# Performance work log

Measured on AMD Instinct MI355X. Metric: run time of the kernel, lower is better.

Reference implementation:

```python
import jax, jax.numpy as jnp
import numpy as np

B, N, D = 1024, 32, 512  # graphs, node types (=nodes per graph), node_dim
EPS = 1e-5

def setup_inputs() -> dict:
    key = jax.random.key(0)
    ks = jax.random.split(key, 6)
    z = jax.random.normal(ks[0], (B, N, D), jnp.float32)
    # each graph contains every node type exactly once, in random order
    idx = jax.vmap(lambda k: jax.random.permutation(k, N))(jax.random.split(ks[1], B)).astype(jnp.int32)
    A = jax.random.normal(ks[2], (N, N), jnp.float32) / np.sqrt(N)
    W1 = jax.random.normal(ks[3], (N, D, 2 * D), jnp.float32) / np.sqrt(D)
    b1 = jnp.zeros((N, 2 * D), jnp.float32)
    W2 = jax.random.normal(ks[4], (N, 2 * D, D), jnp.float32) / np.sqrt(2 * D)
    b2 = jnp.zeros((N, D), jnp.float32)
    gamma = jnp.ones((D,), jnp.float32)
    beta = jnp.zeros((D,), jnp.float32)
    return dict(z=z, idx=idx, A=A, W1=W1, b1=b1, W2=W2, b2=b2, gamma=gamma, beta=beta)

def _layernorm(x, g, b):
    m = jnp.mean(x, axis=-1, keepdims=True)
    v = jnp.var(x, axis=-1, keepdims=True)
    return (x - m) * jax.lax.rsqrt(v + EPS) * g + b

def reference(z, idx, A, W1, b1, W2, b2, gamma, beta):
    # per-graph submatrix of global A: A_sub[b] = A[node_index, node_index]
    A_sub = A[idx[:, :, None], idx[:, None, :]]            # [B,K,K]
    # Az[b] = A_sub[b].T @ z[b]
    Az = jnp.einsum('bkj,bkd->bjd', A_sub, z)              # [B,K,D]
    Az = _layernorm(Az, gamma, beta)
    # route node of type t to expert t: inv[b,t] = position of type t in graph b
    inv = jnp.argsort(idx, axis=1)                         # [B,N]
    x = jnp.take_along_axis(Az, inv[:, :, None], axis=1)   # [B,N,D] type-ordered
    # per-type 2-layer MLP experts (Linear -> ELU -> Linear), dropout in eval mode
    h = jax.nn.elu(jnp.einsum('bnd,ndh->bnh', x, W1) + b1) # [B,N,2D]
    y = jnp.einsum('bnh,nhd->bnd', h, W2) + b2             # [B,N,D]
    # scatter back to node order: node j in graph b has type idx[b,j]
    mix = jnp.take_along_axis(y, idx[:, :, None].astype(jnp.int32), axis=1)
    return mix + Az
```

## Files before the change

### kernel.cpp

```cpp
#include <hip/hip_runtime.h>
#include <hip/hip_bf16.h>
#include <math.h>

#define B_  1024
#define N_  32
#define D_  512
#define EPS_ 1e-5f

typedef __attribute__((ext_vector_type(8))) short bf16x8;
typedef __attribute__((ext_vector_type(4))) float f32x4;
using bf16 = __hip_bfloat16;
typedef unsigned int u32;
typedef const u32 __attribute__((address_space(1)))* gp_t;
typedef u32 __attribute__((address_space(3)))* sp_t;

static __device__ __forceinline__ void gload16(const void* g, void* s) {
  __builtin_amdgcn_global_load_lds((gp_t)g, (sp_t)s, 16, 0, 0);
}
static __device__ __forceinline__ void bar() {
  asm volatile("s_barrier" ::: "memory");
}

static __device__ __forceinline__ unsigned short f2bf(float f) {
  union { float f; u32 u; } c; c.f = f;
  u32 r = c.u + 0x7fff + ((c.u >> 16) & 1);
  return (unsigned short)(r >> 16);
}
static __device__ __forceinline__ float bf2f(unsigned short h) {
  union { u32 u; float f; } c; c.u = ((u32)h) << 16;
  return c.f;
}

__global__ __launch_bounds__(256) void transpose_cast_kernel(
    const float* __restrict__ in, bf16* __restrict__ out, int R, int C) {
  __shared__ unsigned short tile[64][65];
  const size_t mat = (size_t)blockIdx.z * (size_t)R * (size_t)C;
  const float* inp = in + mat;
  bf16* outp = out + mat;
  const int c0 = blockIdx.x * 64, r0 = blockIdx.y * 64;
  const int tr = threadIdx.x >> 4;
  const int tc = (threadIdx.x & 15) * 4;
#pragma unroll
  for (int i = 0; i < 4; ++i) {
    const int r = tr + i * 16;
    float4 v = *(const float4*)&inp[(size_t)(r0 + r) * C + c0 + tc];
    tile[r][tc + 0] = f2bf(v.x);
    tile[r][tc + 1] = f2bf(v.y);
    tile[r][tc + 2] = f2bf(v.z);
    tile[r][tc + 3] = f2bf(v.w);
  }
  __syncthreads();
#pragma unroll
  for (int i = 0; i < 2; ++i) {
    const int chunk = i * 256 + threadIdx.x;
    const int c = chunk >> 3, r8 = (chunk & 7) * 8;
    union { bf16x8 v; unsigned short u[8]; } pk;
#pragma unroll
    for (int k = 0; k < 8; ++k) pk.u[k] = tile[r8 + k][c];
    *(bf16x8*)&outp[(size_t)(c0 + c) * R + r0 + r8] = pk.v;
  }
}

__global__ __launch_bounds__(512) void mix_ln_kernel(
    const float* __restrict__ z, const int* __restrict__ idx,
    const float* __restrict__ A, const float* __restrict__ gamma,
    const float* __restrict__ beta, bf16* __restrict__ x_ws,
    int* __restrict__ inv_ws) {
  __shared__ float As[32][32];
  __shared__ int   p[32];
  __shared__ float red1[8][32];
  __shared__ float red2[8][32];
  __shared__ float meanS[32];
  __shared__ float rstdS[32];

  const int b = blockIdx.x;
  const int t = threadIdx.x;
  const int lane = t & 63, wid = t >> 6;

  if (t < 32) {
    int v = idx[b * 32 + t];
    p[t] = v;
    inv_ws[b * 32 + v] = t;
  }
  __syncthreads();
#pragma unroll
  for (int i = 0; i < 2; ++i) {
    const int id = i * 512 + t;
    As[id >> 5][id & 31] = A[p[id >> 5] * 32 + (id & 31)];
  }
  __syncthreads();

  const float* zb = z + (size_t)b * (N_ * D_) + t;
  float acc[32];
#pragma unroll
  for (int n = 0; n < 32; ++n) acc[n] = 0.f;

  float zr[8];
#pragma unroll 1
  for (int q = 0; q < 4; ++q) {
#pragma unroll
    for (int kk = 0; kk < 8; ++kk) zr[kk] = zb[(q * 8 + kk) * D_];
#pragma unroll
    for (int kk = 0; kk < 8; ++kk) {
      const int k = q * 8 + kk;
      const float zv = zr[kk];
#pragma unroll
      for (int c = 0; c < 8; ++c) {
        float4 a4 = *(const float4*)&As[k][c * 4];
        acc[c * 4 + 0] = fmaf(a4.x, zv, acc[c * 4 + 0]);
        acc[c * 4 + 1] = fmaf(a4.y, zv, acc[c * 4 + 1]);
        acc[c * 4 + 2] = fmaf(a4.z, zv, acc[c * 4 + 2]);
        acc[c * 4 + 3] = fmaf(a4.w, zv, acc[c * 4 + 3]);
      }
    }
  }

#pragma unroll
  for (int n = 0; n < 32; ++n) {
    float v1 = acc[n];
    float v2 = acc[n] * acc[n];
#pragma unroll
    for (int mk = 1; mk < 64; mk <<= 1) {
      v1 += __shfl_xor(v1, mk);
      v2 += __shfl_xor(v2, mk);
    }
    if (lane == 0) { red1[wid][n] = v1; red2[wid][n] = v2; }
  }
  __syncthreads();
  if (t < 32) {
    float S1 = 0.f, S2 = 0.f;
#pragma unroll
    for (int w = 0; w < 8; ++w) { S1 += red1[w][t]; S2 += red2[w][t]; }
    float mean = S1 * (1.f / D_);
    float var  = S2 * (1.f / D_) - mean * mean;
    meanS[t] = mean;
    rstdS[t] = rsqrtf(var + EPS_);
  }
  __syncthreads();

  const float g = gamma[t], be = beta[t];
#pragma unroll
  for (int n = 0; n < 32; ++n) {
    float x0 = (acc[n] - meanS[n]) * rstdS[n] * g + be;
    x_ws[((size_t)n * B_ + b) * D_ + t] = __float2bfloat16(x0);
  }
}

#define STG_A(P, H, S) do {                                                   \
    const bf16* g_ = Ag + (size_t)((H) * 128) * KD + (S) * 64 + soff;         \
    gload16(g_, Alds + (P) * 32768 + (H) * 16384 + dof);                      \
    gload16(g_ + (size_t)64 * KD, Alds + (P) * 32768 + (H) * 16384 + 8192 + dof); \
  } while (0)
#define STG_B(P, H, S) do {                                                   \
    const bf16* g_ = Bg + (size_t)((H) * 128) * KD + (S) * 64 + soff;         \
    gload16(g_, Blds + (P) * 32768 + (H) * 16384 + dof);                      \
    gload16(g_ + (size_t)64 * KD, Blds + (P) * 32768 + (H) * 16384 + 8192 + dof); \
  } while (0)

#define RD_A(P, H) do {                                                       \
    const char* Ab_ = Alds + (P) * 32768 + (H) * 16384;                       \
    _Pragma("unroll")                                                         \
    for (int fi = 0; fi < 2; ++fi) {                                          \
      av[fi][0] = *(const bf16x8*)(Ab_ + raA + fi * 2048 + j16);              \
      av[fi][1] = *(const bf16x8*)(Ab_ + raA + fi * 2048 + (j16 ^ 64));       \
    }                                                                         \
  } while (0)
#define RD_B(P, H, BV) do {                                                   \
    const char* Bb_ = Blds + (P) * 32768 + (H) * 16384;                       \
    _Pragma("unroll")                                                         \
    for (int fj = 0; fj < 4; ++fj) {                                          \
      BV[fj][0] = *(const bf16x8*)(Bb_ + raB + fj * 2048 + j16);              \
      BV[fj][1] = *(const bf16x8*)(Bb_ + raB + fj * 2048 + (j16 ^ 64));       \
    }                                                                         \
  } while (0)

#define MMA16(QR, QC, BV) do {                                                \
    __builtin_amdgcn_s_setprio(1);                                            \
    _Pragma("unroll")                                                         \
    for (int fi = 0; fi < 2; ++fi)                                            \
      _Pragma("unroll")                                                       \
      for (int fj = 0; fj < 4; ++fj) {                                        \
        acc[QR][QC][fi][fj] = __builtin_amdgcn_mfma_f32_16x16x32_bf16(        \
            av[fi][0], BV[fj][0], acc[QR][QC][fi][fj], 0, 0, 0);              \
        acc[QR][QC][fi][fj] = __builtin_amdgcn_mfma_f32_16x16x32_bf16(        \
            av[fi][1], BV[fj][1], acc[QR][QC][fi][fj], 0, 0, 0);              \
      }                                                                       \
    __builtin_amdgcn_s_setprio(0);                                            \
  } while (0)

#define VMC4() asm volatile("s_waitcnt vmcnt(4)" ::: "memory")
#define VMC0() asm volatile("s_waitcnt vmcnt(0)" ::: "memory")

template <int KD, int NS>
static __device__ __forceinline__ void gemm8_core(
    const bf16* __restrict__ Ag, const bf16* __restrict__ Bg,
    char* __restrict__ Alds, char* __restrict__ Blds,
    f32x4 (&acc)[2][2][2][4], const int t) {
  const int lane = t & 63, wid = t >> 6;
  const int llo = lane & 15, lhi = lane >> 4;
  const int raA = ((wid & 3) * 32 + llo) * 128;
  const int raB = ((wid >> 2) * 64 + llo) * 128;
  const int j16 = (lhi ^ (llo & 7)) * 16;
  const int soff = (t >> 3) * KD + ((t ^ (t >> 3)) & 7) * 8;
  const int dof = wid * 1024;

  bf16x8 av[2][2], bv0[4][2], bv1[4][2];

  STG_A(0, 0, 0); STG_B(0, 0, 0); STG_A(0, 1, 0); STG_B(0, 1, 0);
  STG_A(1, 0, 1); STG_B(1, 0, 1);
  VMC4();
  bar();

#pragma unroll 1
  for (int it = 0; it < NS / 2; ++it) {
    const int s0 = 2 * it;
    RD_A(0, 0); RD_B(0, 0, bv0);
    if (s0 + 1 < NS) STG_A(1, 1, s0 + 1);
    bar(); MMA16(0, 0, bv0); bar();
    RD_B(0, 1, bv1);
    if (s0 + 1 < NS) STG_B(1, 1, s0 + 1);
    bar(); MMA16(0, 1, bv1); bar();
    RD_A(0, 1);
    if (s0 + 2 < NS) STG_A(0, 0, s0 + 2);
    bar(); MMA16(1, 1, bv1); bar();
    if (s0 + 2 < NS) STG_B(0, 0, s0 + 2);
    bar(); MMA16(1, 0, bv0);
    if (s0 + 2 < NS) { VMC4(); } else { VMC0(); }
    bar();
    const int s1 = s0 + 1;
    RD_A(1, 0); RD_B(1, 0, bv0);
    if (s1 + 1 < NS) STG_A(0, 1, s1 + 1);
    bar(); MMA16(0, 0, bv0); bar();
    RD_B(1, 1, bv1);
    if (s1 + 1 < NS) STG_B(0, 1, s1 + 1);
    bar(); MMA16(0, 1, bv1); bar();
    RD_A(1, 1);
    if (s1 + 2 < NS) STG_A(1, 0, s1 + 2);
    bar(); MMA16(1, 1, bv1); bar();
    if (s1 + 2 < NS) STG_B(1, 0, s1 + 2);
    bar(); MMA16(1, 0, bv0);
    if (s1 + 2 < NS) { VMC4(); } else { VMC0(); }
    bar();
  }
}

__global__ __launch_bounds__(512, 2) void gemm1_kernel(
    const bf16* __restrict__ X,
    const bf16* __restrict__ W1t,
    const float* __restrict__ b1,
    bf16* __restrict__ Hout) {
  extern __shared__ char lds[];
  char* Alds = lds;
  char* Blds = lds + 65536;

  const int bid = blockIdx.x;
  const int swz = (bid & 7) * 64 + (bid >> 3);
  const int m  = swz >> 4;
  const int r_ = swz & 15;
  const int hb = r_ >> 2, bb = r_ & 3;

  const int t = threadIdx.x;
  const int lane = t & 63, wid = t >> 6;
  const int llo = lane & 15, lhi = lane >> 4;

  const bf16* Ag = W1t + (size_t)m * (1024 * 512) + (size_t)(hb * 256) * 512;
  const bf16* Bg = X   + (size_t)m * (1024 * 512) + (size_t)(bb * 256) * 512;

  const f32x4 fzero = {0.f, 0.f, 0.f, 0.f};
  f32x4 acc[2][2][2][4];
#pragma unroll
  for (int a = 0; a < 2; ++a)
#pragma unroll
    for (int b = 0; b < 2; ++b)
#pragma unroll
      for (int c = 0; c < 2; ++c)
#pragma unroll
        for (int d = 0; d < 4; ++d) acc[a][b][c][d] = fzero;

  gemm8_core<512, 8>(Ag, Bg, Alds, Blds, acc, t);

  const float* b1m = b1 + m * 1024 + hb * 256;
#pragma unroll
  for (int qr = 0; qr < 2; ++qr)
#pragma unroll
    for (int fi = 0; fi < 2; ++fi) {
      const int h_loc = qr * 128 + (wid & 3) * 32 + fi * 16 + lhi * 4;
      const float4 bi = *(const float4*)&b1m[h_loc];
#pragma unroll
      for (int qc = 0; qc < 2; ++qc)
#pragma unroll
        for (int fj = 0; fj < 4; ++fj) {
          const int b_loc = qc * 128 + (wid >> 2) * 64 + fj * 16 + llo;
          float v0 = acc[qr][qc][fi][fj][0] + bi.x;
          float v1 = acc[qr][qc][fi][fj][1] + bi.y;
          float v2 = acc[qr][qc][fi][fj][2] + bi.z;
          float v3 = acc[qr][qc][fi][fj][3] + bi.w;
          v0 = v0 > 0.f ? v0 : __expf(v0) - 1.0f;
          v1 = v1 > 0.f ? v1 : __expf(v1) - 1.0f;
          v2 = v2 > 0.f ? v2 : __expf(v2) - 1.0f;
          v3 = v3 > 0.f ? v3 : __expf(v3) - 1.0f;
          ushort4 pk;
          pk.x = f2bf(v0); pk.y = f2bf(v1); pk.z = f2bf(v2); pk.w = f2bf(v3);
          const int byte = (b_loc * 512 + h_loc * 2) ^ ((b_loc & 7) << 4);
          *(ushort4*)(lds + byte) = pk;
        }
    }
  __syncthreads();
  bf16* Hm = Hout + (size_t)m * (1024 * 1024);
  const int b0 = bb * 256, h0 = hb * 256;
#pragma unroll
  for (int r = 0; r < 16; ++r) {
    const int chunk = r * 512 + t;
    const int bl = chunk >> 5, hc = chunk & 31;
    const int byte = (bl * 512 + hc * 16) ^ ((bl & 7) << 4);
    bf16x8 v = *(const bf16x8*)(lds + byte);
    *(bf16x8*)&Hm[(size_t)(b0 + bl) * 1024 + h0 + hc * 8] = v;
  }
}

__global__ __launch_bounds__(512, 2) void gemm2_kernel(
    const bf16* __restrict__ Hin,
    const bf16* __restrict__ W2t,
    const float* __restrict__ b2,
    const bf16* __restrict__ Xb,
    const int* __restrict__ inv,
    float* __restrict__ out) {
  extern __shared__ char lds[];
  char* Alds = lds;
  char* Blds = lds + 65536;

  const int bid = blockIdx.x;
  const int swz = (bid & 7) * 32 + (bid >> 3);
  const int m  = swz >> 3;
  const int r_ = swz & 7;
  const int db_ = r_ >> 2, bb = r_ & 3;

  const int t = threadIdx.x;
  const int lane = t & 63, wid = t >> 6;
  const int llo = lane & 15, lhi = lane >> 4;

  const bf16* Ag = W2t + (size_t)m * (512 * 1024) + (size_t)(db_ * 256) * 1024;
  const bf16* Bg = Hin + (size_t)m * (1024 * 1024) + (size_t)(bb * 256) * 1024;

  const f32x4 fzero = {0.f, 0.f, 0.f, 0.f};
  f32x4 acc[2][2][2][4];
#pragma unroll
  for (int a = 0; a < 2; ++a)
#pragma unroll
    for (int b = 0; b < 2; ++b)
#pragma unroll
      for (int c = 0; c < 2; ++c)
#pragma unroll
        for (int d = 0; d < 4; ++d) acc[a][b][c][d] = fzero;

  gemm8_core<1024, 16>(Ag, Bg, Alds, Blds, acc, t);

  const float* b2m = b2 + m * 512;
  const bf16* Xm = Xb + (size_t)m * (1024 * 512);
#pragma unroll
  for (int qc = 0; qc < 2; ++qc)
#pragma unroll
    for (int fj = 0; fj < 4; ++fj) {
      const int b_ = bb * 256 + qc * 128 + (wid >> 2) * 64 + fj * 16 + llo;
      const int n_out = inv[b_ * 32 + m];
      float* orow = out + ((size_t)b_ * 32 + n_out) * 512;
      const bf16* xrow = Xm + (size_t)b_ * 512;
#pragma unroll
      for (int qr = 0; qr < 2; ++qr)
#pragma unroll
        for (int fi = 0; fi < 2; ++fi) {
          const int d0 = db_ * 256 + qr * 128 + (wid & 3) * 32 + fi * 16 + lhi * 4;
          const float4 bi = *(const float4*)&b2m[d0];
          const ushort4 xr = *(const ushort4*)&xrow[d0];
          float4 v;
          v.x = acc[qr][qc][fi][fj][0] + bi.x + bf2f(xr.x);
          v.y = acc[qr][qc][fi][fj][1] + bi.y + bf2f(xr.y);
          v.z = acc[qr][qc][fi][fj][2] + bi.z + bf2f(xr.z);
          v.w = acc[qr][qc][fi][fj][3] + bi.w + bf2f(xr.w);
          *(float4*)&orow[d0] = v;
        }
    }
}

extern "C" void kernel_launch(void* const* d_in, const int* in_sizes, int n_in,
                              void* d_out, int out_size, void* d_ws, size_t ws_size,
                              hipStream_t stream) {
  const float* z     = (const float*)d_in[0];
  const int*   idx   = (const int*)d_in[1];
  const float* A     = (const float*)d_in[2];
  const float* W1    = (const float*)d_in[3];
  const float* b1    = (const float*)d_in[4];
  const float* W2    = (const float*)d_in[5];
  const float* b2    = (const float*)d_in[6];
  const float* gamma = (const float*)d_in[7];
  const float* beta  = (const float*)d_in[8];
  float* out = (float*)d_out;
  char* ws = (char*)d_ws;

  const size_t OFF_X   = 0;
  const size_t OFF_H   = 33554432;
  const size_t OFF_W1T = 100663296;
  const size_t OFF_W2T = 134217728;
  const size_t OFF_INV = 167772160;
  const size_t NEED    = 167903232;
  if (ws_size < NEED) return;

  bf16* Xb  = (bf16*)(ws + OFF_X);
  bf16* Hb  = (bf16*)(ws + OFF_H);
  bf16* W1t = (bf16*)(ws + OFF_W1T);
  bf16* W2t = (bf16*)(ws + OFF_W2T);
  int*  inv = (int*)(ws + OFF_INV);

  hipFuncSetAttribute((const void*)gemm1_kernel,
                      hipFuncAttributeMaxDynamicSharedMemorySize, 131072);
  hipFuncSetAttribute((const void*)gemm2_kernel,
                      hipFuncAttributeMaxDynamicSharedMemorySize, 131072);

  transpose_cast_kernel<<<dim3(16, 8, 32), 256, 0, stream>>>(W1, W1t, 512, 1024);
  transpose_cast_kernel<<<dim3(8, 16, 32), 256, 0, stream>>>(W2, W2t, 1024, 512);

  mix_ln_kernel<<<dim3(B_), 512, 0, stream>>>(z, idx, A, gamma, beta, Xb, inv);

  gemm1_kernel<<<dim3(512), 512, 131072, stream>>>(Xb, W1t, b1, Hb);
  gemm2_kernel<<<dim3(256), 512, 131072, stream>>>(Hb, W2t, b2, Xb, inv, out);
}
```

Before: 199.8 us.

## Compute graph mixing matmul in mix_ln kernel with bf16 MFMA

Replaces the per-thread scalar FMA loop computing A_sub^T @ z with 16x16x32 bf16 MFMA instructions, and halves the block size to 256 threads. Each thread now handles a 16-wide column tile across 8 d-tiles. The LayerNorm reductions are restructured around the MFMA output layout. This cuts FMA work and shuffle reductions in the mixing stage, but rounds A and z to bf16 before the matmul, which lowers accuracy. Stores become scattered 2-byte writes instead of fully coalesced ones.

```diff
diff --git a/kernel.cpp b/kernel.cpp
--- a/kernel.cpp
+++ b/kernel.cpp
@@ -61,21 +61,22 @@
   }
 }
 
-__global__ __launch_bounds__(512) void mix_ln_kernel(
+__global__ __launch_bounds__(256) void mix_ln_kernel(
     const float* __restrict__ z, const int* __restrict__ idx,
     const float* __restrict__ A, const float* __restrict__ gamma,
     const float* __restrict__ beta, bf16* __restrict__ x_ws,
     int* __restrict__ inv_ws) {
   __shared__ float As[32][32];
   __shared__ int   p[32];
-  __shared__ float red1[8][32];
-  __shared__ float red2[8][32];
+  __shared__ float red1[4][32];
+  __shared__ float red2[4][32];
   __shared__ float meanS[32];
   __shared__ float rstdS[32];
 
   const int b = blockIdx.x;
   const int t = threadIdx.x;
   const int lane = t & 63, wid = t >> 6;
+  const int llo = lane & 15, lhi = lane >> 4;
 
   if (t < 32) {
     int v = idx[b * 32 + t];
@@ -84,53 +85,81 @@
   }
   __syncthreads();
 #pragma unroll
-  for (int i = 0; i < 2; ++i) {
-    const int id = i * 512 + t;
+  for (int i = 0; i < 4; ++i) {
+    const int id = i * 256 + t;
     As[id >> 5][id & 31] = A[p[id >> 5] * 32 + (id & 31)];
   }
   __syncthreads();
 
-  const float* zb = z + (size_t)b * (N_ * D_) + t;
-  float acc[32];
-#pragma unroll
-  for (int n = 0; n < 32; ++n) acc[n] = 0.f;
-
-  float zr[8];
-#pragma unroll 1
-  for (int q = 0; q < 4; ++q) {
-#pragma unroll
-    for (int kk = 0; kk < 8; ++kk) zr[kk] = zb[(q * 8 + kk) * D_];
-#pragma unroll
-    for (int kk = 0; kk < 8; ++kk) {
-      const int k = q * 8 + kk;
-      const float zv = zr[kk];
-#pragma unroll
-      for (int c = 0; c < 8; ++c) {
-        float4 a4 = *(const float4*)&As[k][c * 4];
-        acc[c * 4 + 0] = fmaf(a4.x, zv, acc[c * 4 + 0]);
-        acc[c * 4 + 1] = fmaf(a4.y, zv, acc[c * 4 + 1]);
-        acc[c * 4 + 2] = fmaf(a4.z, zv, acc[c * 4 + 2]);
-        acc[c * 4 + 3] = fmaf(a4.w, zv, acc[c * 4 + 3]);
+  bf16x8 af[2];
+#pragma unroll
+  for (int nt = 0; nt < 2; ++nt) {
+    union { bf16x8 v; unsigned short s[8]; } u;
+#pragma unroll
+    for (int j = 0; j < 8; ++j)
+      u.s[j] = f2bf(As[lhi * 8 + j][nt * 16 + llo]);
+    af[nt] = u.v;
+  }
+
+  const float* zb = z + (size_t)b * (N_ * D_) + (size_t)(lhi * 8) * D_ + llo;
+  const f32x4 fz = {0.f, 0.f, 0.f, 0.f};
+  f32x4 acc[2][8];
+#pragma unroll
+  for (int nt = 0; nt < 2; ++nt)
+#pragma unroll
+    for (int dt = 0; dt < 8; ++dt) acc[nt][dt] = fz;
+
+#pragma unroll
+  for (int h = 0; h < 2; ++h) {
+    float zr[4][8];
+#pragma unroll
+    for (int dd = 0; dd < 4; ++dd)
+#pragma unroll
+      for (int j = 0; j < 8; ++j)
+        zr[dd][j] = zb[j * D_ + ((wid * 8 + h * 4 + dd) * 16)];
+#pragma unroll
+    for (int dd = 0; dd < 4; ++dd) {
+      const int dt = h * 4 + dd;
+      union { bf16x8 v; unsigned short s[8]; } u;
+#pragma unroll
+      for (int j = 0; j < 8; ++j) u.s[j] = f2bf(zr[dd][j]);
+      acc[0][dt] = __builtin_amdgcn_mfma_f32_16x16x32_bf16(af[0], u.v, acc[0][dt], 0, 0, 0);
+      acc[1][dt] = __builtin_amdgcn_mfma_f32_16x16x32_bf16(af[1], u.v, acc[1][dt], 0, 0, 0);
+    }
+  }
+
+  float s1[2][4], s2[2][4];
+#pragma unroll
+  for (int nt = 0; nt < 2; ++nt)
+#pragma unroll
+    for (int r = 0; r < 4; ++r) {
+      float a = 0.f, q = 0.f;
+#pragma unroll
+      for (int dt = 0; dt < 8; ++dt) {
+        float v = acc[nt][dt][r];
+        a += v; q += v * v;
       }
+#pragma unroll
+      for (int mk = 1; mk < 16; mk <<= 1) {
+        a += __shfl_xor(a, mk);
+        q += __shfl_xor(q, mk);
+      }
+      s1[nt][r] = a; s2[nt][r] = q;
     }
-  }
-
-#pragma unroll
-  for (int n = 0; n < 32; ++n) {
-    float v1 = acc[n];
-    float v2 = acc[n] * acc[n];
-#pragma unroll
-    for (int mk = 1; mk < 64; mk <<= 1) {
-      v1 += __shfl_xor(v1, mk);
-      v2 += __shfl_xor(v2, mk);
-    }
-    if (lane == 0) { red1[wid][n] = v1; red2[wid][n] = v2; }
+  if (llo == 0) {
+#pragma unroll
+    for (int nt = 0; nt < 2; ++nt)
+#pragma unroll
+      for (int r = 0; r < 4; ++r) {
+        const int n = nt * 16 + lhi * 4 + r;
+        red1[wid][n] = s1[nt][r];
+        red2[wid][n] = s2[nt][r];
+      }
   }
   __syncthreads();
   if (t < 32) {
-    float S1 = 0.f, S2 = 0.f;
-#pragma unroll
-    for (int w = 0; w < 8; ++w) { S1 += red1[w][t]; S2 += red2[w][t]; }
+    float S1 = red1[0][t] + red1[1][t] + red1[2][t] + red1[3][t];
+    float S2 = red2[0][t] + red2[1][t] + red2[2][t] + red2[3][t];
     float mean = S1 * (1.f / D_);
     float var  = S2 * (1.f / D_) - mean * mean;
     meanS[t] = mean;
@@ -138,12 +167,26 @@
   }
   __syncthreads();
 
-  const float g = gamma[t], be = beta[t];
-#pragma unroll
-  for (int n = 0; n < 32; ++n) {
-    float x0 = (acc[n] - meanS[n]) * rstdS[n] * g + be;
-    x_ws[((size_t)n * B_ + b) * D_ + t] = __float2bfloat16(x0);
-  }
+  float gv[8], bev[8];
+#pragma unroll
+  for (int dt = 0; dt < 8; ++dt) {
+    const int d = (wid * 8 + dt) * 16 + llo;
+    gv[dt] = gamma[d]; bev[dt] = beta[d];
+  }
+#pragma unroll
+  for (int nt = 0; nt < 2; ++nt)
+#pragma unroll
+    for (int r = 0; r < 4; ++r) {
+      const int n = nt * 16 + lhi * 4 + r;
+      const float mn = meanS[n], rs = rstdS[n];
+      unsigned short* xrow = (unsigned short*)(x_ws + ((size_t)n * B_ + b) * D_);
+#pragma unroll
+      for (int dt = 0; dt < 8; ++dt) {
+        const int d = (wid * 8 + dt) * 16 + llo;
+        float v = (acc[nt][dt][r] - mn) * rs * gv[dt] + bev[dt];
+        xrow[d] = f2bf(v);
+      }
+    }
 }
 
 #define STG_A(P, H, S) do {                                                   \
@@ -419,7 +462,7 @@
   transpose_cast_kernel<<<dim3(16, 8, 32), 256, 0, stream>>>(W1, W1t, 512, 1024);
   transpose_cast_kernel<<<dim3(8, 16, 32), 256, 0, stream>>>(W2, W2t, 1024, 512);
 
-  mix_ln_kernel<<<dim3(B_), 512, 0, stream>>>(z, idx, A, gamma, beta, Xb, inv);
+  mix_ln_kernel<<<dim3(B_), 256, 0, stream>>>(z, idx, A, gamma, beta, Xb, inv);
 
   gemm1_kernel<<<dim3(512), 512, 131072, stream>>>(Xb, W1t, b1, Hb);
   gemm2_kernel<<<dim3(256), 512, 131072, stream>>>(Hb, W2t, b2, Xb, inv, out);
```

After: 168.5 us. 1.19x faster.
